# Kernel tuning notes

Hardware: AMD Instinct MI355X
Metric: run time of the kernel (lower is better)

## Reference

```python
import jax, jax.numpy as jnp
import numpy as np

NUM_HEADS = 16
HEAD_DIM = 64


def setup_inputs() -> dict:
    key = jax.random.key(0)
    k1, k2, k3 = jax.random.split(key, 3)
    dim = NUM_HEADS * HEAD_DIM  # 1024
    x = jax.random.normal(k1, (1, 4096, dim), dtype=jnp.float32)
    w_qkv = jax.random.normal(k2, (dim, 3 * dim), dtype=jnp.float32) * (dim ** -0.5)
    w_out = jax.random.normal(k3, (dim, dim), dtype=jnp.float32) * (dim ** -0.5)
    b_out = jnp.zeros((dim,), dtype=jnp.float32)
    return {"x": x, "w_qkv": w_qkv, "w_out": w_out, "b_out": b_out}


def reference(x, w_qkv, w_out, b_out):
    b, n, dim = x.shape
    h, d = NUM_HEADS, HEAD_DIM
    qkv = x @ w_qkv                                  # [b, n, 3*h*d]
    q, k, v = jnp.split(qkv, 3, axis=-1)
    q = q.reshape(b, n, h, d)
    k = k.reshape(b, n, h, d)
    v = v.reshape(b, n, h, d)  # NOTE: unused below — source module's bug uses K as V
    q = q * (d ** -0.5)
    # The chunked online-softmax in the source is mathematically exact softmax
    # attention; express it directly. Scores layout matches einsum '...qhd,...khd->...qhk'.
    scores = jnp.einsum('bqhd,bkhd->bqhk', q, k)     # [b, n, h, n]
    attn = jax.nn.softmax(scores, axis=-1)
    # Faithful to source bug: value_chunk was sliced from `key`, so V := K here.
    att = jnp.einsum('bqhk,bkhd->bqhd', attn, k)     # [b, n, h, d]
    out = att.reshape(b, n, h * d)
    return out @ w_out + b_out
```

## Files before the change

### kernel.cpp

```cpp
#include <hip/hip_runtime.h>
#include <hip/hip_bf16.h>

#define NT 4096
#define DIM 1024
#define NH 16
#define HD 64

typedef __attribute__((ext_vector_type(8))) short bf16x8;
typedef __attribute__((ext_vector_type(4))) float f32x4;
typedef __attribute__((ext_vector_type(16))) float f32x16;

__device__ __forceinline__ unsigned short f2b(float f) {
  union { float f; unsigned u; } v; v.f = f;
  unsigned r = v.u + 0x7fffu + ((v.u >> 16) & 1u);
  return (unsigned short)(r >> 16);
}
__device__ __forceinline__ float b2f(unsigned short u) {
  union { unsigned u; float f; } v; v.u = ((unsigned)u) << 16; return v.f;
}

__device__ __forceinline__ float fexp2(float x) {
#if __has_builtin(__builtin_amdgcn_exp2f)
  return __builtin_amdgcn_exp2f(x);
#else
  return exp2f(x);
#endif
}

__global__ void k_cvt(const float4* __restrict__ src, ushort4* __restrict__ dst, int n4) {
  int i = blockIdx.x * blockDim.x + threadIdx.x;
  if (i >= n4) return;
  float4 v = src[i];
  ushort4 o;
  o.x = f2b(v.x); o.y = f2b(v.y); o.z = f2b(v.z); o.w = f2b(v.w);
  dst[i] = o;
}

__global__ __launch_bounds__(256) void k_trans_w(const float* __restrict__ src, int S,
                                                 unsigned short* __restrict__ dst, int Kdim) {
  __shared__ float tile[32][33];
  int j0 = blockIdx.x * 32, k0 = blockIdx.y * 32;
  int t = threadIdx.x;
  int c = t & 31, rq = t >> 5;
#pragma unroll
  for (int i = 0; i < 4; i++) {
    int r = rq + i * 8;
    tile[r][c] = src[(size_t)(k0 + r) * S + j0 + c];
  }
  __syncthreads();
#pragma unroll
  for (int i = 0; i < 4; i++) {
    int jr = rq + i * 8;
    dst[(size_t)(j0 + jr) * Kdim + k0 + c] = f2b(tile[c][jr]);
  }
}

template <int EPI>
__global__ __launch_bounds__(256) void k_gemm(const unsigned short* __restrict__ A,
                                              const unsigned short* __restrict__ Bt,
                                              unsigned short* __restrict__ qh,
                                              unsigned short* __restrict__ krm,
                                              float* __restrict__ cout,
                                              const float* __restrict__ bias) {
  __shared__ unsigned short As[128][40];
  __shared__ unsigned short Bs[128][40];
  const int K = 1024;
  int m0 = blockIdx.y * 128, n0 = blockIdx.x * 128;
  int t = threadIdx.x;
  int w = t >> 6, l = t & 63;
  int wr = w >> 1, wc = w & 1;
  int lq = l & 15, lg = l >> 4;
  f32x4 zero = {0.f, 0.f, 0.f, 0.f};
  f32x4 acc[4][4];
#pragma unroll
  for (int i = 0; i < 4; i++)
#pragma unroll
    for (int j = 0; j < 4; j++) acc[i][j] = zero;

  for (int k0 = 0; k0 < K; k0 += 32) {
#pragma unroll
    for (int s = 0; s < 2; s++) {
      int slot = t + s * 256;
      int r = slot >> 2, c8 = (slot & 3) * 8;
      *reinterpret_cast<bf16x8*>(&As[r][c8]) =
          *reinterpret_cast<const bf16x8*>(A + (size_t)(m0 + r) * K + k0 + c8);
      *reinterpret_cast<bf16x8*>(&Bs[r][c8]) =
          *reinterpret_cast<const bf16x8*>(Bt + (size_t)(n0 + r) * K + k0 + c8);
    }
    __syncthreads();
    bf16x8 af[4], bf[4];
#pragma unroll
    for (int mi = 0; mi < 4; mi++)
      af[mi] = *reinterpret_cast<bf16x8*>(&As[wr * 64 + mi * 16 + lq][lg * 8]);
#pragma unroll
    for (int ni = 0; ni < 4; ni++)
      bf[ni] = *reinterpret_cast<bf16x8*>(&Bs[wc * 64 + ni * 16 + lq][lg * 8]);
#pragma unroll
    for (int mi = 0; mi < 4; mi++)
#pragma unroll
      for (int ni = 0; ni < 4; ni++)
        acc[mi][ni] =
            __builtin_amdgcn_mfma_f32_16x16x32_bf16(af[mi], bf[ni], acc[mi][ni], 0, 0, 0);
    __syncthreads();
  }
#pragma unroll
  for (int mi = 0; mi < 4; mi++) {
#pragma unroll
    for (int ni = 0; ni < 4; ni++) {
      int j = n0 + wc * 64 + ni * 16 + lq;
#pragma unroll
      for (int r = 0; r < 4; r++) {
        int row = m0 + wr * 64 + mi * 16 + lg * 4 + r;
        float v = acc[mi][ni][r];
        if (EPI == 0) {
          if (j < DIM) {
            qh[((size_t)(j >> 6) << 18) + (size_t)row * HD + (j & 63)] =
                f2b(v * 0.18033688011112042f);
          } else {
            int jj = j - DIM;
            krm[((size_t)(jj >> 6) << 18) + (size_t)row * HD + (jj & 63)] = f2b(v);
          }
        } else {
          cout[(size_t)row * DIM + j] = v + bias[j];
        }
      }
    }
  }
}

__global__ __launch_bounds__(256) void k_transK(const unsigned short* __restrict__ krm,
                                                unsigned short* __restrict__ kt) {
  __shared__ unsigned short tile[64][72];
  int h = blockIdx.y, n0 = blockIdx.x * 64;
  int t = threadIdx.x;
  const unsigned short* src = krm + (size_t)h * NT * HD;
#pragma unroll
  for (int s = 0; s < 2; s++) {
    int slot = t + s * 256;
    int r = slot >> 3, c8 = (slot & 7) * 8;
    *reinterpret_cast<bf16x8*>(&tile[r][c8]) =
        *reinterpret_cast<const bf16x8*>(src + (size_t)(n0 + r) * HD + c8);
  }
  __syncthreads();
  unsigned short* dst = kt + (size_t)h * HD * NT;
#pragma unroll
  for (int s = 0; s < 2; s++) {
    int slot = t + s * 256;
    int dd = slot & 63, c8 = (slot >> 6) * 8;
    bf16x8 vv;
#pragma unroll
    for (int i = 0; i < 8; i++) vv[i] = (short)tile[c8 + i][dd];
    *reinterpret_cast<bf16x8*>(dst + (size_t)dd * NT + n0 + c8) = vv;
  }
}

__global__ __launch_bounds__(256, 4) void k_attn(const unsigned short* __restrict__ qh,
                                                 const unsigned short* __restrict__ krm,
                                                 const unsigned short* __restrict__ kt,
                                                 unsigned short* __restrict__ part0,
                                                 unsigned short* __restrict__ part1,
                                                 float* __restrict__ stats) {
  __shared__ __align__(16) unsigned char sbuf[2][16384];

  int hw = blockIdx.x;
  int xcd = hw & 7, idx = hw >> 3;
  int h = xcd * 2 + (idx >> 6);
  int sub = idx & 63;
  int q0 = (sub & 31) * 128;
  int kvs = sub >> 5;
  int kv_base = kvs * (NT / 2);

  unsigned short* ob = kvs ? part1 : part0;
  float* mb = stats + (size_t)kvs * 2 * (NH * NT);
  float* lb = mb + NH * NT;

  int t = threadIdx.x, w = t >> 6, l = t & 63;
  int lq = l & 31, hi = l >> 5;
  const unsigned char* Kb = (const unsigned char*)(krm + (size_t)h * NT * HD);
  const unsigned char* Tb = (const unsigned char*)(kt + (size_t)h * HD * NT);
  const unsigned short* Qb = qh + (size_t)h * NT * HD;

  int qrow = q0 + w * 32 + lq;
  bf16x8 qf[4];
#pragma unroll
  for (int ds = 0; ds < 4; ds++)
    qf[ds] = *reinterpret_cast<const bf16x8*>(Qb + (size_t)qrow * HD + ds * 16 + hi * 8);

  int rdbase = lq * 16 + hi * 1024;

  f32x16 o0, o1;
#pragma unroll
  for (int r = 0; r < 16; r++) { o0[r] = 0.f; o1[r] = 0.f; }
  float m_run = -3.0e38f, l_run = 0.f;

  auto STAGE = [&](int b, int kv0) {
    unsigned char* base = &sbuf[b][0];
#pragma unroll
    for (int i = 0; i < 4; i++) {
      int c = w * 4 + i;
      const unsigned char* g;
      if (c < 8) {
        g = Kb + (size_t)(kv0 + l) * 128 + (c >> 1) * 32 + (c & 1) * 16;
      } else {
        g = Tb + (size_t)l * 8192 + (size_t)kv0 * 2 + (c - 8) * 16;
      }
      __builtin_amdgcn_global_load_lds(
          (const __attribute__((address_space(1))) unsigned int*)g,
          (__attribute__((address_space(3))) unsigned int*)(base + c * 1024), 16, 0, 0);
    }
  };

  STAGE(0, kv_base);
  __syncthreads();

  for (int tile = 0; tile < 32; tile++) {
    int cur = tile & 1;
    if (tile < 31) STAGE(cur ^ 1, kv_base + (tile + 1) * 64);
    const unsigned char* KaB = &sbuf[cur][0];

    f32x16 s0, s1;
#pragma unroll
    for (int r = 0; r < 16; r++) { s0[r] = 0.f; s1[r] = 0.f; }
#pragma unroll
    for (int ds = 0; ds < 4; ds++) {
      bf16x8 a0 = *reinterpret_cast<const bf16x8*>(KaB + rdbase + ds * 2048);
      bf16x8 a1 = *reinterpret_cast<const bf16x8*>(KaB + rdbase + ds * 2048 + 512);
      s0 = __builtin_amdgcn_mfma_f32_32x32x16_bf16(a0, qf[ds], s0, 0, 0, 0);
      s1 = __builtin_amdgcn_mfma_f32_32x32x16_bf16(a1, qf[ds], s1, 0, 0, 0);
    }

    float pm = -3.0e38f;
#pragma unroll
    for (int r = 0; r < 16; r++) pm = fmaxf(pm, fmaxf(s0[r], s1[r]));
    pm = fmaxf(pm, __shfl_xor(pm, 32));
    if (__any(pm > m_run + 8.0f)) {
      float newm = fmaxf(m_run, pm);
      float al = fexp2(m_run - newm);
#pragma unroll
      for (int r = 0; r < 16; r++) {
        float av = __shfl(al, (r & 3) + 8 * (r >> 2) + 4 * hi);
        o0[r] *= av;
        o1[r] *= av;
      }
      l_run *= al;
      m_run = newm;
    }
    float ps = 0.f;
#pragma unroll
    for (int r = 0; r < 16; r++) { s0[r] = fexp2(s0[r] - m_run); ps += s0[r]; }
#pragma unroll
    for (int r = 0; r < 16; r++) { s1[r] = fexp2(s1[r] - m_run); ps += s1[r]; }
    ps += __shfl_xor(ps, 32);
    l_run += ps;

    unsigned pk0[8], pk1[8];
#pragma unroll
    for (int i = 0; i < 8; i++) {
      asm("v_cvt_pk_bf16_f32 %0, %1, %2" : "=v"(pk0[i]) : "v"(s0[2 * i]), "v"(s0[2 * i + 1]));
      asm("v_cvt_pk_bf16_f32 %0, %1, %2" : "=v"(pk1[i]) : "v"(s1[2 * i]), "v"(s1[2 * i + 1]));
    }
    bf16x8 pf[4];
#pragma unroll
    for (int kb = 0; kb < 4; kb++) {
      const unsigned* pk = (kb < 2) ? pk0 : pk1;
      int m = kb & 1;
      unsigned d0 = pk[4 * m + 0], d1 = pk[4 * m + 1];
      unsigned e0 = pk[4 * m + 2], e1 = pk[4 * m + 3];
      asm volatile("v_permlane32_swap_b32 %0, %1" : "+v"(d0), "+v"(e0));
      asm volatile("v_permlane32_swap_b32 %0, %1" : "+v"(d1), "+v"(e1));
      union { unsigned u[4]; bf16x8 v; } uu;
      uu.u[0] = d0; uu.u[1] = d1; uu.u[2] = e0; uu.u[3] = e1;
      pf[kb] = uu.v;
    }

#pragma unroll
    for (int kb = 0; kb < 4; kb++) {
      bf16x8 v0 = *reinterpret_cast<const bf16x8*>(KaB + rdbase + 8192 + kb * 2048);
      o0 = __builtin_amdgcn_mfma_f32_32x32x16_bf16(pf[kb], v0, o0, 0, 0, 0);
    }
#pragma unroll
    for (int kb = 0; kb < 4; kb++) {
      bf16x8 v1 = *reinterpret_cast<const bf16x8*>(KaB + rdbase + 8192 + kb * 2048 + 512);
      o1 = __builtin_amdgcn_mfma_f32_32x32x16_bf16(pf[kb], v1, o1, 0, 0, 0);
    }
    __syncthreads();
  }

#pragma unroll
  for (int r = 0; r < 16; r++) {
    int qr = (r & 3) + 8 * (r >> 2) + 4 * hi;
    size_t grow = (size_t)(q0 + w * 32 + qr);
    ob[grow * DIM + h * HD + lq] = f2b(o0[r]);
    ob[grow * DIM + h * HD + 32 + lq] = f2b(o1[r]);
  }
  if (l < 32) {
    int q = q0 + w * 32 + lq;
    mb[h * NT + q] = m_run;
    lb[h * NT + q] = l_run;
  }
}

__global__ __launch_bounds__(256) void k_combine(unsigned short* __restrict__ p0b,
                                                 const unsigned short* __restrict__ p1b,
                                                 const float* __restrict__ stats) {
  int i = blockIdx.x * 256 + threadIdx.x;
  int base = i * 8;
  int q = base >> 10;
  int c = base & 1023;
  int h = c >> 6;
  const float* m0 = stats;
  const float* l0 = stats + NH * NT;
  const float* m1 = stats + 2 * NH * NT;
  const float* l1 = stats + 3 * NH * NT;
  float mm0 = m0[h * NT + q], ll0 = l0[h * NT + q];
  float mm1 = m1[h * NT + q], ll1 = l1[h * NT + q];
  float M = fmaxf(mm0, mm1);
  float s0 = fexp2(mm0 - M), s1 = fexp2(mm1 - M);
  float dn = ll0 * s0 + ll1 * s1;
  float a0 = s0 / dn, a1 = s1 / dn;
  bf16x8 v0 = *reinterpret_cast<const bf16x8*>(p0b + base);
  bf16x8 v1 = *reinterpret_cast<const bf16x8*>(p1b + base);
  bf16x8 o;
#pragma unroll
  for (int j = 0; j < 8; j++)
    o[j] = (short)f2b(b2f((unsigned short)v0[j]) * a0 + b2f((unsigned short)v1[j]) * a1);
  *reinterpret_cast<bf16x8*>(p0b + base) = o;
}

extern "C" void kernel_launch(void* const* d_in, const int* in_sizes, int n_in,
                              void* d_out, int out_size, void* d_ws, size_t ws_size,
                              hipStream_t stream) {
  const float* x = (const float*)d_in[0];
  const float* w_qkv = (const float*)d_in[1];
  const float* w_out = (const float*)d_in[2];
  const float* b_out = (const float*)d_in[3];
  float* out = (float*)d_out;

  char* ws = (char*)d_ws;
  unsigned short* xb   = (unsigned short*)(ws);
  unsigned short* wqkT = (unsigned short*)(ws + 8388608);
  unsigned short* woT  = (unsigned short*)(ws + 12582912);
  unsigned short* qhb  = (unsigned short*)(ws + 14680064);
  unsigned short* krm  = (unsigned short*)(ws + 23068672);
  unsigned short* ktb  = (unsigned short*)(ws + 31457280);
  unsigned short* attb = (unsigned short*)(ws + 39845888);
  float* stats = (float*)wqkT;

  k_cvt<<<(NT * DIM / 4 + 255) / 256, 256, 0, stream>>>((const float4*)x, (ushort4*)xb,
                                                        NT * DIM / 4);
  dim3 g1(2048 / 32, 1024 / 32);
  k_trans_w<<<g1, 256, 0, stream>>>(w_qkv, 3 * DIM, wqkT, DIM);
  dim3 g2(1024 / 32, 1024 / 32);
  k_trans_w<<<g2, 256, 0, stream>>>(w_out, DIM, woT, DIM);
  dim3 g3(2048 / 128, NT / 128);
  k_gemm<0><<<g3, 256, 0, stream>>>(xb, wqkT, qhb, krm, nullptr, nullptr);
  dim3 g4(NT / 64, NH);
  k_transK<<<g4, 256, 0, stream>>>(krm, ktb);
  k_attn<<<(NT / 128) * NH * 2, 256, 0, stream>>>(qhb, krm, ktb, attb, xb, stats);
  k_combine<<<NT * DIM / 8 / 256, 256, 0, stream>>>(attb, xb, stats);
  dim3 g5(DIM / 128, NT / 128);
  k_gemm<1><<<g5, 256, 0, stream>>>(attb, woT, nullptr, nullptr, out, b_out);
}
```

Before: 181.0 us.

## Use async global-to-LDS swizzled loads in GEMM and MFMA row-sum in attention

The GEMM's padded shared tiles become unpadded XOR-swizzled buffers filled directly with global_load_lds, so staging no longer goes through registers. In attention, the softmax row sum is now computed by an extra MFMA against a vector of bf16 ones, replacing the VALU adds and the cross-lane shuffle. The row-max reduction is split into four independent chains to shorten the dependency chain. In exchange, the row sum is taken from bf16-rounded probabilities, and each tile costs four extra MFMAs plus another accumulator register set.

```diff
diff --git a/kernel.cpp b/kernel.cpp
--- a/kernel.cpp
+++ b/kernel.cpp
@@ -62,14 +62,16 @@
                                               unsigned short* __restrict__ krm,
                                               float* __restrict__ cout,
                                               const float* __restrict__ bias) {
-  __shared__ unsigned short As[128][40];
-  __shared__ unsigned short Bs[128][40];
+  __shared__ __align__(16) unsigned short As[4096];
+  __shared__ __align__(16) unsigned short Bs[4096];
   const int K = 1024;
   int m0 = blockIdx.y * 128, n0 = blockIdx.x * 128;
   int t = threadIdx.x;
   int w = t >> 6, l = t & 63;
   int wr = w >> 1, wc = w & 1;
   int lq = l & 15, lg = l >> 4;
+  char* AsB = (char*)As;
+  char* BsB = (char*)Bs;
   f32x4 zero = {0.f, 0.f, 0.f, 0.f};
   f32x4 acc[4][4];
 #pragma unroll
@@ -80,21 +82,31 @@
   for (int k0 = 0; k0 < K; k0 += 32) {
 #pragma unroll
     for (int s = 0; s < 2; s++) {
-      int slot = t + s * 256;
-      int r = slot >> 2, c8 = (slot & 3) * 8;
-      *reinterpret_cast<bf16x8*>(&As[r][c8]) =
-          *reinterpret_cast<const bf16x8*>(A + (size_t)(m0 + r) * K + k0 + c8);
-      *reinterpret_cast<bf16x8*>(&Bs[r][c8]) =
-          *reinterpret_cast<const bf16x8*>(Bt + (size_t)(n0 + r) * K + k0 + c8);
+      int slot = s * 256 + t;
+      int row = slot >> 2;
+      int cc = (slot & 3) ^ ((row >> 1) & 3);
+      int db = (s * 256 + (t & 192)) * 16;
+      const unsigned short* ga = A + (size_t)(m0 + row) * K + k0 + cc * 8;
+      const unsigned short* gb = Bt + (size_t)(n0 + row) * K + k0 + cc * 8;
+      __builtin_amdgcn_global_load_lds(
+          (const __attribute__((address_space(1))) unsigned int*)ga,
+          (__attribute__((address_space(3))) unsigned int*)(AsB + db), 16, 0, 0);
+      __builtin_amdgcn_global_load_lds(
+          (const __attribute__((address_space(1))) unsigned int*)gb,
+          (__attribute__((address_space(3))) unsigned int*)(BsB + db), 16, 0, 0);
     }
     __syncthreads();
     bf16x8 af[4], bf[4];
 #pragma unroll
-    for (int mi = 0; mi < 4; mi++)
-      af[mi] = *reinterpret_cast<bf16x8*>(&As[wr * 64 + mi * 16 + lq][lg * 8]);
-#pragma unroll
-    for (int ni = 0; ni < 4; ni++)
-      bf[ni] = *reinterpret_cast<bf16x8*>(&Bs[wc * 64 + ni * 16 + lq][lg * 8]);
+    for (int mi = 0; mi < 4; mi++) {
+      int row = wr * 64 + mi * 16 + lq;
+      af[mi] = *reinterpret_cast<bf16x8*>(AsB + row * 64 + ((lg ^ ((row >> 1) & 3)) * 16));
+    }
+#pragma unroll
+    for (int ni = 0; ni < 4; ni++) {
+      int row = wc * 64 + ni * 16 + lq;
+      bf[ni] = *reinterpret_cast<bf16x8*>(BsB + row * 64 + ((lg ^ ((row >> 1) & 3)) * 16));
+    }
 #pragma unroll
     for (int mi = 0; mi < 4; mi++)
 #pragma unroll
@@ -186,12 +198,16 @@
   for (int ds = 0; ds < 4; ds++)
     qf[ds] = *reinterpret_cast<const bf16x8*>(Qb + (size_t)qrow * HD + ds * 16 + hi * 8);
 
+  bf16x8 ones;
+#pragma unroll
+  for (int i = 0; i < 8; i++) ones[i] = (short)0x3F80;
+
   int rdbase = lq * 16 + hi * 1024;
 
-  f32x16 o0, o1;
-#pragma unroll
-  for (int r = 0; r < 16; r++) { o0[r] = 0.f; o1[r] = 0.f; }
-  float m_run = -3.0e38f, l_run = 0.f;
+  f32x16 o0, o1, lacc;
+#pragma unroll
+  for (int r = 0; r < 16; r++) { o0[r] = 0.f; o1[r] = 0.f; lacc[r] = 0.f; }
+  float m_run = -3.0e38f;
 
   auto STAGE = [&](int b, int kv0) {
     unsigned char* base = &sbuf[b][0];
@@ -229,9 +245,16 @@
       s1 = __builtin_amdgcn_mfma_f32_32x32x16_bf16(a1, qf[ds], s1, 0, 0, 0);
     }
 
-    float pm = -3.0e38f;
-#pragma unroll
-    for (int r = 0; r < 16; r++) pm = fmaxf(pm, fmaxf(s0[r], s1[r]));
+    float pa = fmaxf(s0[0], s1[0]), pb = fmaxf(s0[1], s1[1]);
+    float pc = fmaxf(s0[2], s1[2]), pd = fmaxf(s0[3], s1[3]);
+#pragma unroll
+    for (int r = 4; r < 16; r += 4) {
+      pa = fmaxf(pa, fmaxf(s0[r], s1[r]));
+      pb = fmaxf(pb, fmaxf(s0[r + 1], s1[r + 1]));
+      pc = fmaxf(pc, fmaxf(s0[r + 2], s1[r + 2]));
+      pd = fmaxf(pd, fmaxf(s0[r + 3], s1[r + 3]));
+    }
+    float pm = fmaxf(fmaxf(pa, pb), fmaxf(pc, pd));
     pm = fmaxf(pm, __shfl_xor(pm, 32));
     if (__any(pm > m_run + 8.0f)) {
       float newm = fmaxf(m_run, pm);
@@ -241,17 +264,14 @@
         float av = __shfl(al, (r & 3) + 8 * (r >> 2) + 4 * hi);
         o0[r] *= av;
         o1[r] *= av;
+        lacc[r] *= av;
       }
-      l_run *= al;
       m_run = newm;
     }
-    float ps = 0.f;
-#pragma unroll
-    for (int r = 0; r < 16; r++) { s0[r] = fexp2(s0[r] - m_run); ps += s0[r]; }
-#pragma unroll
-    for (int r = 0; r < 16; r++) { s1[r] = fexp2(s1[r] - m_run); ps += s1[r]; }
-    ps += __shfl_xor(ps, 32);
-    l_run += ps;
+#pragma unroll
+    for (int r = 0; r < 16; r++) s0[r] = fexp2(s0[r] - m_run);
+#pragma unroll
+    for (int r = 0; r < 16; r++) s1[r] = fexp2(s1[r] - m_run);
 
     unsigned pk0[8], pk1[8];
 #pragma unroll
@@ -283,6 +303,9 @@
       bf16x8 v1 = *reinterpret_cast<const bf16x8*>(KaB + rdbase + 8192 + kb * 2048 + 512);
       o1 = __builtin_amdgcn_mfma_f32_32x32x16_bf16(pf[kb], v1, o1, 0, 0, 0);
     }
+#pragma unroll
+    for (int kb = 0; kb < 4; kb++)
+      lacc = __builtin_amdgcn_mfma_f32_32x32x16_bf16(pf[kb], ones, lacc, 0, 0, 0);
     __syncthreads();
   }
 
@@ -293,10 +316,14 @@
     ob[grow * DIM + h * HD + lq] = f2b(o0[r]);
     ob[grow * DIM + h * HD + 32 + lq] = f2b(o1[r]);
   }
-  if (l < 32) {
-    int q = q0 + w * 32 + lq;
-    mb[h * NT + q] = m_run;
-    lb[h * NT + q] = l_run;
+#pragma unroll
+  for (int r = 0; r < 16; r++) {
+    int qr = (r & 3) + 8 * (r >> 2) + 4 * hi;
+    if (lq == qr) {
+      int q = q0 + w * 32 + qr;
+      mb[h * NT + q] = m_run;
+      lb[h * NT + q] = lacc[r];
+    }
   }
 }
 
```

Result: no change. 178.4 us (-1.4%).
